# Kernel tuning notes

Hardware: AMD Instinct MI355X
Metric: run time of the kernel (lower is better)

Reference implementation:

```python
import jax, jax.numpy as jnp
import numpy as np

N_SEGMENT = 16
N_HEADS = 12
DIM = 768
HEAD_DIM = DIM // N_HEADS
LN_EPS = 1e-5


def setup_inputs() -> dict:
    key = jax.random.key(0)
    ks = jax.random.split(key, 12)
    nt, p, c = 512, 197, DIM
    s = 1.0 / np.sqrt(c)
    return {
        "x": jax.random.normal(ks[0], (nt, p, c), dtype=jnp.float32),
        "w1": jax.random.uniform(ks[1], (1, 1, c), dtype=jnp.float32) * 2.0 - 1.0,
        "ln_g": jnp.ones((c,), dtype=jnp.float32),
        "ln_b": jnp.zeros((c,), dtype=jnp.float32),
        "Wq": jax.random.normal(ks[2], (c, c), dtype=jnp.float32) * s,
        "bq": jax.random.normal(ks[3], (c,), dtype=jnp.float32) * 0.02,
        "Wk": jax.random.normal(ks[4], (c, c), dtype=jnp.float32) * s,
        "bk": jax.random.normal(ks[5], (c,), dtype=jnp.float32) * 0.02,
        "Wv": jax.random.normal(ks[6], (c, c), dtype=jnp.float32) * s,
        "bv": jax.random.normal(ks[7], (c,), dtype=jnp.float32) * 0.02,
        "Wo": jax.random.normal(ks[8], (c, c), dtype=jnp.float32) * s,
        "bo": jax.random.normal(ks[9], (c,), dtype=jnp.float32) * 0.02,
    }


def _layer_norm(x, g, b):
    mu = jnp.mean(x, axis=-1, keepdims=True)
    var = jnp.mean(jnp.square(x - mu), axis=-1, keepdims=True)
    return (x - mu) * jax.lax.rsqrt(var + LN_EPS) * g + b


def _attention(h, Wq, bq, Wk, bk, Wv, bv, Wo, bo):
    # h: [B, T, C]
    B, T, C = h.shape
    def heads(y):
        return y.reshape(B, T, N_HEADS, HEAD_DIM).transpose(0, 2, 1, 3)
    q = heads(h @ Wq + bq)  # [B, H, T, Dh]
    k = heads(h @ Wk + bk)
    v = heads(h @ Wv + bv)
    scores = jnp.einsum("bhtd,bhsd->bhts", q, k) / jnp.sqrt(jnp.float32(HEAD_DIM))
    probs = jax.nn.softmax(scores, axis=-1)
    ctx = jnp.einsum("bhts,bhsd->bhtd", probs, v)
    ctx = ctx.transpose(0, 2, 1, 3).reshape(B, T, C)
    return ctx @ Wo + bo


def reference(x, w1, ln_g, ln_b, Wq, bq, Wk, bk, Wv, bv, Wo, bo):
    nt, p, c = x.shape
    B = nt // N_SEGMENT
    xr = x.reshape(B, N_SEGMENT, p, c)
    s = xr[:, :, 0]  # CLS tokens [B, T, C]
    # weighted temporal shift (in torch this mutates the view; residual sees it)
    s_shift = s.at[:, 1:].add(s[:, :-1] * w1)
    t = _layer_norm(s_shift, ln_g, ln_b)
    t = _attention(t, Wq, bq, Wk, bk, Wv, bv, Wo, bo)
    t = t + s_shift  # residual uses SHIFTED tokens (aliasing in torch source)
    out = xr.at[:, :, 0].set(t)
    return out.reshape(nt, p, c)
```

## Files before the change

### kernel.cpp

```cpp
#include <hip/hip_runtime.h>
#include <math.h>

typedef __attribute__((ext_vector_type(8))) short short8;
typedef __attribute__((ext_vector_type(4))) float f32x4;
typedef __attribute__((ext_vector_type(4))) unsigned short us4;

constexpr int NSEG = 16;
constexpr int CC   = 768;
constexpr int PP   = 197;
constexpr int NH   = 12;
constexpr int HD   = 64;
constexpr int NT   = 512;
constexpr int MN   = NT * CC;
constexpr float LN_EPS = 1e-5f;

constexpr unsigned CPT  = 196 * CC / 4;
constexpr unsigned TOK4 = PP * CC / 4;
constexpr unsigned ROW4 = CC / 4;
constexpr unsigned W4TOT = (unsigned)NT * CPT;

__device__ inline unsigned short f2bf(float f) {
    unsigned u = __float_as_uint(f);
    u += 0x7fffu + ((u >> 16) & 1u);
    return (unsigned short)(u >> 16);
}

__device__ inline void copy_slice(const float* __restrict__ x, float* __restrict__ out,
                                  unsigned start, unsigned end,
                                  unsigned gthread, unsigned nthreads) {
    const float4* __restrict__ x4 = (const float4*)x;
    float4* __restrict__ o4 = (float4*)out;
    for (unsigned i = start + gthread; i < end; i += nthreads) {
        unsigned t = i / CPT;
        unsigned w = i - t * CPT;
        unsigned idx = t * TOK4 + ROW4 + w;
        o4[idx] = x4[idx];
    }
}

template<bool ADD_RES>
__device__ inline void gemm_tile(const unsigned short* __restrict__ A,
                                 const unsigned short* __restrict__ Bt,
                                 const float* __restrict__ bias,
                                 const float* __restrict__ res,
                                 float* __restrict__ outp,
                                 int by, int bx, size_t orow) {
    int tid  = threadIdx.x;
    int lane = tid & 63, wv = tid >> 6;
    int wr = wv >> 1, wc = wv & 1;
    int l15 = lane & 15, lh = lane >> 4;
    int m0 = by * 64 + wr * 32;
    int n0 = bx * 64 + wc * 32;
    f32x4 acc[2][2] = {};
    const unsigned short* Ar0 = A  + (size_t)(m0 + l15) * CC + lh * 8;
    const unsigned short* Ar1 = Ar0 + 16 * CC;
    const unsigned short* Br0 = Bt + (size_t)(n0 + l15) * CC + lh * 8;
    const unsigned short* Br1 = Br0 + 16 * CC;
    #pragma unroll 4
    for (int k0 = 0; k0 < CC; k0 += 32) {
        short8 a0 = *(const short8*)(Ar0 + k0);
        short8 a1 = *(const short8*)(Ar1 + k0);
        short8 b0 = *(const short8*)(Br0 + k0);
        short8 b1 = *(const short8*)(Br1 + k0);
        acc[0][0] = __builtin_amdgcn_mfma_f32_16x16x32_bf16(a0, b0, acc[0][0], 0, 0, 0);
        acc[0][1] = __builtin_amdgcn_mfma_f32_16x16x32_bf16(a0, b1, acc[0][1], 0, 0, 0);
        acc[1][0] = __builtin_amdgcn_mfma_f32_16x16x32_bf16(a1, b0, acc[1][0], 0, 0, 0);
        acc[1][1] = __builtin_amdgcn_mfma_f32_16x16x32_bf16(a1, b1, acc[1][1], 0, 0, 0);
    }
    #pragma unroll
    for (int mf = 0; mf < 2; ++mf)
        #pragma unroll
        for (int nf = 0; nf < 2; ++nf)
            #pragma unroll
            for (int r = 0; r < 4; ++r) {
                int row = m0 + mf * 16 + lh * 4 + r;
                int col = n0 + nf * 16 + l15;
                float v = acc[mf][nf][r] + bias[col];
                if (ADD_RES) v += res[(size_t)row * CC + col];
                outp[(size_t)row * orow + col] = v;
            }
}

constexpr int K1_LN = NT, K1_CVT = 2304, K1_CPY = 768;
__global__ __launch_bounds__(256) void k1(const float* __restrict__ x, const float* __restrict__ w1,
        const float* __restrict__ g, const float* __restrict__ bln,
        const float* __restrict__ Wq, const float* __restrict__ Wk,
        const float* __restrict__ Wv, const float* __restrict__ Wo,
        float* __restrict__ s_shift, unsigned short* __restrict__ tln,
        unsigned short* __restrict__ wt, float* __restrict__ out,
        unsigned cstart, unsigned cend) {
    __shared__ float smem[32 * 33];
    int bid = blockIdx.x, tid = threadIdx.x;
    if (bid < K1_LN) {
        int r = bid, seg = r & (NSEG - 1);
        float vals[3]; float local = 0.f;
        #pragma unroll
        for (int i = 0; i < 3; ++i) {
            int c = tid + i * 256;
            float v = x[(size_t)r * PP * CC + c];
            if (seg > 0) v += w1[c] * x[(size_t)(r - 1) * PP * CC + c];
            vals[i] = v; local += v;
        }
        smem[tid] = local; __syncthreads();
        for (int off = 128; off > 0; off >>= 1) {
            if (tid < off) smem[tid] += smem[tid + off];
            __syncthreads();
        }
        float mu = smem[0] * (1.0f / CC); __syncthreads();
        float lv = 0.f;
        #pragma unroll
        for (int i = 0; i < 3; ++i) { float d = vals[i] - mu; lv += d * d; }
        smem[tid] = lv; __syncthreads();
        for (int off = 128; off > 0; off >>= 1) {
            if (tid < off) smem[tid] += smem[tid + off];
            __syncthreads();
        }
        float rstd = rsqrtf(smem[0] * (1.0f / CC) + LN_EPS);
        #pragma unroll
        for (int i = 0; i < 3; ++i) {
            int c = tid + i * 256;
            s_shift[(size_t)r * CC + c] = vals[i];
            tln[(size_t)r * CC + c] = f2bf((vals[i] - mu) * rstd * g[c] + bln[c]);
        }
    } else if (bid < K1_LN + K1_CVT) {
        int idx = bid - K1_LN;
        int mat = idx / 576, tile = idx % 576;
        int tr = tile / 24, tc = tile % 24;
        const float* W = mat == 0 ? Wq : mat == 1 ? Wk : mat == 2 ? Wv : Wo;
        int lr = tid >> 3, lc = (tid & 7) * 4;
        float4 v = *(const float4*)(W + (size_t)(tr * 32 + lr) * CC + tc * 32 + lc);
        smem[lr * 33 + lc + 0] = v.x; smem[lr * 33 + lc + 1] = v.y;
        smem[lr * 33 + lc + 2] = v.z; smem[lr * 33 + lc + 3] = v.w;
        __syncthreads();
        int ln_ = tid >> 3, kc = (tid & 7) * 4;
        us4 o;
        #pragma unroll
        for (int j = 0; j < 4; ++j) o[j] = f2bf(smem[(kc + j) * 33 + ln_]);
        *(us4*)(wt + (size_t)mat * CC * CC + (size_t)(tc * 32 + ln_) * CC + tr * 32 + kc) = o;
    } else {
        unsigned cb = bid - (K1_LN + K1_CVT);
        copy_slice(x, out, cstart, cend, cb * 256 + tid, K1_CPY * 256);
    }
}

constexpr int K2_GEMM = 288, K2_CPY = 1024;
__global__ __launch_bounds__(256) void k2(const unsigned short* __restrict__ tln,
        const unsigned short* __restrict__ wt,
        const float* __restrict__ bq, const float* __restrict__ bk, const float* __restrict__ bv,
        float* __restrict__ qkv,
        const float* __restrict__ x, float* __restrict__ out,
        unsigned cstart, unsigned cend) {
    int bid = blockIdx.x, tid = threadIdx.x;
    if (bid < K2_GEMM) {
        int z = bid / 96, rem = bid % 96;
        int by = rem / 12, bx = rem % 12;
        const unsigned short* Bt = wt + (size_t)z * CC * CC;
        const float* bias = z == 0 ? bq : (z == 1 ? bk : bv);
        float* outp = qkv + (size_t)z * MN;
        gemm_tile<false>(tln, Bt, bias, nullptr, outp, by, bx, CC);
    } else {
        unsigned cb = bid - K2_GEMM;
        copy_slice(x, out, cstart, cend, cb * 256 + tid, K2_CPY * 256);
    }
}

constexpr int K3_ATT = 32 * NH, K3_CPY = 1024;
__global__ __launch_bounds__(256) void k3(const float* __restrict__ qkv,
        unsigned short* __restrict__ ctxb,
        const float* __restrict__ x, float* __restrict__ out,
        unsigned cstart, unsigned cend) {
    int bid = blockIdx.x, tid = threadIdx.x;
    if (bid < K3_ATT) {
        const float* q = qkv;
        const float* k = qkv + MN;
        const float* v = qkv + 2 * MN;
        int bb = bid / NH, h = bid % NH;
        __shared__ float qs[16][HD], ks[16][HD], vs[16][HD];
        __shared__ float sc[16][17];
        __shared__ float rsum[16];
        for (int i = tid; i < 16 * HD; i += 256) {
            int t = i >> 6, d = i & 63;
            size_t gidx = (size_t)(bb * NSEG + t) * CC + h * HD + d;
            qs[t][d] = q[gidx]; ks[t][d] = k[gidx]; vs[t][d] = v[gidx];
        }
        __syncthreads();
        {
            int t = tid >> 4, s = tid & 15;
            float acc = 0.f;
            #pragma unroll
            for (int d = 0; d < HD; ++d) acc += qs[t][d] * ks[s][d];
            sc[t][s] = acc * 0.125f;
        }
        __syncthreads();
        if (tid < 16) {
            float m = -1e30f;
            #pragma unroll
            for (int s = 0; s < 16; ++s) m = fmaxf(m, sc[tid][s]);
            float sum = 0.f;
            #pragma unroll
            for (int s = 0; s < 16; ++s) { float e = __expf(sc[tid][s] - m); sc[tid][s] = e; sum += e; }
            rsum[tid] = sum;
        }
        __syncthreads();
        for (int i = tid; i < 16 * HD; i += 256) {
            int t = i >> 6, d = i & 63;
            float acc = 0.f;
            #pragma unroll
            for (int s = 0; s < 16; ++s) acc += sc[t][s] * vs[s][d];
            ctxb[(size_t)(bb * NSEG + t) * CC + h * HD + d] = f2bf(acc / rsum[t]);
        }
    } else {
        unsigned cb = bid - K3_ATT;
        copy_slice(x, out, cstart, cend, cb * 256 + tid, K3_CPY * 256);
    }
}

constexpr int K4_GEMM = 96, K4_CPY = 1024;
__global__ __launch_bounds__(256) void k4(const unsigned short* __restrict__ ctxb,
        const unsigned short* __restrict__ wto,
        const float* __restrict__ bo, const float* __restrict__ s_shift,
        float* __restrict__ out, const float* __restrict__ x,
        unsigned cstart, unsigned cend) {
    int bid = blockIdx.x, tid = threadIdx.x;
    if (bid < K4_GEMM) {
        int by = bid / 12, bx = bid % 12;
        gemm_tile<true>(ctxb, wto, bo, s_shift, out, by, bx, (size_t)PP * CC);
    } else {
        unsigned cb = bid - K4_GEMM;
        copy_slice(x, out, cstart, cend, cb * 256 + tid, K4_CPY * 256);
    }
}

extern "C" void kernel_launch(void* const* d_in, const int* in_sizes, int n_in,
                              void* d_out, int out_size, void* d_ws, size_t ws_size,
                              hipStream_t stream) {
    const float* x    = (const float*)d_in[0];
    const float* w1   = (const float*)d_in[1];
    const float* ln_g = (const float*)d_in[2];
    const float* ln_b = (const float*)d_in[3];
    const float* Wq   = (const float*)d_in[4];
    const float* bq   = (const float*)d_in[5];
    const float* Wk   = (const float*)d_in[6];
    const float* bk   = (const float*)d_in[7];
    const float* Wv   = (const float*)d_in[8];
    const float* bv   = (const float*)d_in[9];
    const float* Wo   = (const float*)d_in[10];
    const float* bo   = (const float*)d_in[11];
    float* out = (float*)d_out;

    float* ws      = (float*)d_ws;
    float* s_shift = ws;
    float* qkv     = s_shift + MN;
    unsigned short* tln  = (unsigned short*)(qkv + 3 * MN);
    unsigned short* ctxb = tln + MN;
    unsigned short* wt   = ctxb + MN;

    const unsigned s0 = 0, s1 = 5400000u, s2 = 10400000u, s3 = 15400000u, s4 = W4TOT;

    k1<<<K1_LN + K1_CVT + K1_CPY, 256, 0, stream>>>(x, w1, ln_g, ln_b, Wq, Wk, Wv, Wo,
                                                    s_shift, tln, wt, out, s0, s1);
    k2<<<K2_GEMM + K2_CPY, 256, 0, stream>>>(tln, wt, bq, bk, bv, qkv, x, out, s1, s2);
    k3<<<K3_ATT + K3_CPY, 256, 0, stream>>>(qkv, ctxb, x, out, s2, s3);
    k4<<<K4_GEMM + K4_CPY, 256, 0, stream>>>(ctxb, wt + (size_t)3 * CC * CC, bo, s_shift,
                                             out, x, s3, s4);
}
```

Baseline: 159.7 us.

## Fuse attention with output projection, store QKV in bf16, rebalance copy across three kernels

Attention and the output projection are merged into one kernel. Each of 32 blocks computes all heads for one batch with wave-level softmax, then runs a per-block MFMA GEMM against Wo. This drops the fourth launch. Q/K/V are now stored as bf16 instead of fp32 to cut intermediate traffic, and weight conversion is done by 576 blocks that each handle all four matrices. The bulk patch-token copy is split into fixed per-block chunks spread over three 2048-block kernels, with occupancy hints in launch bounds. The risks are that the output GEMM now runs on only 32 blocks and that bf16 QKV lowers precision.

```diff
diff --git a/kernel.cpp b/kernel.cpp
--- a/kernel.cpp
+++ b/kernel.cpp
@@ -15,83 +15,45 @@
 constexpr float LN_EPS = 1e-5f;
 
 constexpr unsigned CPT  = 196 * CC / 4;
-constexpr unsigned TOK4 = PP * CC / 4;
 constexpr unsigned ROW4 = CC / 4;
 constexpr unsigned W4TOT = (unsigned)NT * CPT;
+
+constexpr unsigned Q1 = 2944, S1 = 0;
+constexpr unsigned Q2 = 3248, S2 = S1 + 2048u * Q1;
+constexpr unsigned Q3 = 3216, S3 = S2 + 2048u * Q2;
 
 __device__ inline unsigned short f2bf(float f) {
     unsigned u = __float_as_uint(f);
     u += 0x7fffu + ((u >> 16) & 1u);
     return (unsigned short)(u >> 16);
 }
-
-__device__ inline void copy_slice(const float* __restrict__ x, float* __restrict__ out,
-                                  unsigned start, unsigned end,
-                                  unsigned gthread, unsigned nthreads) {
-    const float4* __restrict__ x4 = (const float4*)x;
-    float4* __restrict__ o4 = (float4*)out;
-    for (unsigned i = start + gthread; i < end; i += nthreads) {
-        unsigned t = i / CPT;
-        unsigned w = i - t * CPT;
-        unsigned idx = t * TOK4 + ROW4 + w;
-        o4[idx] = x4[idx];
-    }
-}
-
-template<bool ADD_RES>
-__device__ inline void gemm_tile(const unsigned short* __restrict__ A,
-                                 const unsigned short* __restrict__ Bt,
-                                 const float* __restrict__ bias,
-                                 const float* __restrict__ res,
-                                 float* __restrict__ outp,
-                                 int by, int bx, size_t orow) {
-    int tid  = threadIdx.x;
-    int lane = tid & 63, wv = tid >> 6;
-    int wr = wv >> 1, wc = wv & 1;
-    int l15 = lane & 15, lh = lane >> 4;
-    int m0 = by * 64 + wr * 32;
-    int n0 = bx * 64 + wc * 32;
-    f32x4 acc[2][2] = {};
-    const unsigned short* Ar0 = A  + (size_t)(m0 + l15) * CC + lh * 8;
-    const unsigned short* Ar1 = Ar0 + 16 * CC;
-    const unsigned short* Br0 = Bt + (size_t)(n0 + l15) * CC + lh * 8;
-    const unsigned short* Br1 = Br0 + 16 * CC;
-    #pragma unroll 4
-    for (int k0 = 0; k0 < CC; k0 += 32) {
-        short8 a0 = *(const short8*)(Ar0 + k0);
-        short8 a1 = *(const short8*)(Ar1 + k0);
-        short8 b0 = *(const short8*)(Br0 + k0);
-        short8 b1 = *(const short8*)(Br1 + k0);
-        acc[0][0] = __builtin_amdgcn_mfma_f32_16x16x32_bf16(a0, b0, acc[0][0], 0, 0, 0);
-        acc[0][1] = __builtin_amdgcn_mfma_f32_16x16x32_bf16(a0, b1, acc[0][1], 0, 0, 0);
-        acc[1][0] = __builtin_amdgcn_mfma_f32_16x16x32_bf16(a1, b0, acc[1][0], 0, 0, 0);
-        acc[1][1] = __builtin_amdgcn_mfma_f32_16x16x32_bf16(a1, b1, acc[1][1], 0, 0, 0);
-    }
-    #pragma unroll
-    for (int mf = 0; mf < 2; ++mf)
-        #pragma unroll
-        for (int nf = 0; nf < 2; ++nf)
-            #pragma unroll
-            for (int r = 0; r < 4; ++r) {
-                int row = m0 + mf * 16 + lh * 4 + r;
-                int col = n0 + nf * 16 + l15;
-                float v = acc[mf][nf][r] + bias[col];
-                if (ADD_RES) v += res[(size_t)row * CC + col];
-                outp[(size_t)row * orow + col] = v;
-            }
-}
-
-constexpr int K1_LN = NT, K1_CVT = 2304, K1_CPY = 768;
-__global__ __launch_bounds__(256) void k1(const float* __restrict__ x, const float* __restrict__ w1,
+__device__ inline float bf2f(short v) {
+    return __uint_as_float((unsigned)(unsigned short)v << 16);
+}
+__device__ inline unsigned cidx(unsigned i) {
+    unsigned t = i / CPT;
+    return i + t * ROW4 + ROW4;
+}
+
+__device__ inline void copy_blk(const float* __restrict__ xf, float* __restrict__ of,
+                                unsigned rbeg, unsigned rend, int tid) {
+    const f32x4* __restrict__ x4 = (const f32x4*)xf;
+    f32x4* __restrict__ o4 = (f32x4*)of;
+    for (unsigned i = rbeg + tid; i < rend; i += 256) {
+        unsigned a = cidx(i);
+        o4[a] = x4[a];
+    }
+}
+
+__global__ __launch_bounds__(256, 8) void k1(const float* __restrict__ x, const float* __restrict__ w1,
         const float* __restrict__ g, const float* __restrict__ bln,
         const float* __restrict__ Wq, const float* __restrict__ Wk,
         const float* __restrict__ Wv, const float* __restrict__ Wo,
         float* __restrict__ s_shift, unsigned short* __restrict__ tln,
-        unsigned short* __restrict__ wt, float* __restrict__ out,
-        unsigned cstart, unsigned cend) {
+        unsigned short* __restrict__ wt, float* __restrict__ out) {
     __shared__ float smem[32 * 33];
     int bid = blockIdx.x, tid = threadIdx.x;
-    if (bid < K1_LN) {
+    if (bid < NT) {
         int r = bid, seg = r & (NSEG - 1);
         float vals[3]; float local = 0.f;
         #pragma unroll
@@ -122,113 +84,162 @@
             s_shift[(size_t)r * CC + c] = vals[i];
             tln[(size_t)r * CC + c] = f2bf((vals[i] - mu) * rstd * g[c] + bln[c]);
         }
-    } else if (bid < K1_LN + K1_CVT) {
-        int idx = bid - K1_LN;
-        int mat = idx / 576, tile = idx % 576;
-        int tr = tile / 24, tc = tile % 24;
-        const float* W = mat == 0 ? Wq : mat == 1 ? Wk : mat == 2 ? Wv : Wo;
-        int lr = tid >> 3, lc = (tid & 7) * 4;
-        float4 v = *(const float4*)(W + (size_t)(tr * 32 + lr) * CC + tc * 32 + lc);
-        smem[lr * 33 + lc + 0] = v.x; smem[lr * 33 + lc + 1] = v.y;
-        smem[lr * 33 + lc + 2] = v.z; smem[lr * 33 + lc + 3] = v.w;
-        __syncthreads();
-        int ln_ = tid >> 3, kc = (tid & 7) * 4;
-        us4 o;
-        #pragma unroll
-        for (int j = 0; j < 4; ++j) o[j] = f2bf(smem[(kc + j) * 33 + ln_]);
-        *(us4*)(wt + (size_t)mat * CC * CC + (size_t)(tc * 32 + ln_) * CC + tr * 32 + kc) = o;
-    } else {
-        unsigned cb = bid - (K1_LN + K1_CVT);
-        copy_slice(x, out, cstart, cend, cb * 256 + tid, K1_CPY * 256);
-    }
-}
-
-constexpr int K2_GEMM = 288, K2_CPY = 1024;
-__global__ __launch_bounds__(256) void k2(const unsigned short* __restrict__ tln,
+    } else if (bid < NT + 576) {
+        int bi = bid - NT;
+        int tr = bi / 24, tc = bi % 24;
+        #pragma unroll
+        for (int rep = 0; rep < 4; ++rep) {
+            const float* W = rep == 0 ? Wq : rep == 1 ? Wk : rep == 2 ? Wv : Wo;
+            int lr = tid >> 3, lc = (tid & 7) * 4;
+            float4 v = *(const float4*)(W + (size_t)(tr * 32 + lr) * CC + tc * 32 + lc);
+            smem[lr * 33 + lc + 0] = v.x; smem[lr * 33 + lc + 1] = v.y;
+            smem[lr * 33 + lc + 2] = v.z; smem[lr * 33 + lc + 3] = v.w;
+            __syncthreads();
+            int ln_ = tid >> 3, kc = (tid & 7) * 4;
+            us4 o;
+            #pragma unroll
+            for (int j = 0; j < 4; ++j) o[j] = f2bf(smem[(kc + j) * 33 + ln_]);
+            *(us4*)(wt + (size_t)rep * CC * CC + (size_t)(tc * 32 + ln_) * CC + tr * 32 + kc) = o;
+            __syncthreads();
+        }
+    }
+    copy_blk(x, out, S1 + (unsigned)bid * Q1, S1 + (unsigned)(bid + 1) * Q1, tid);
+}
+
+__global__ __launch_bounds__(256, 4) void k2(const unsigned short* __restrict__ tln,
         const unsigned short* __restrict__ wt,
         const float* __restrict__ bq, const float* __restrict__ bk, const float* __restrict__ bv,
-        float* __restrict__ qkv,
-        const float* __restrict__ x, float* __restrict__ out,
-        unsigned cstart, unsigned cend) {
+        unsigned short* __restrict__ qkvb,
+        const float* __restrict__ x, float* __restrict__ out) {
     int bid = blockIdx.x, tid = threadIdx.x;
-    if (bid < K2_GEMM) {
+    if (bid < 288) {
         int z = bid / 96, rem = bid % 96;
         int by = rem / 12, bx = rem % 12;
         const unsigned short* Bt = wt + (size_t)z * CC * CC;
         const float* bias = z == 0 ? bq : (z == 1 ? bk : bv);
-        float* outp = qkv + (size_t)z * MN;
-        gemm_tile<false>(tln, Bt, bias, nullptr, outp, by, bx, CC);
-    } else {
-        unsigned cb = bid - K2_GEMM;
-        copy_slice(x, out, cstart, cend, cb * 256 + tid, K2_CPY * 256);
-    }
-}
-
-constexpr int K3_ATT = 32 * NH, K3_CPY = 1024;
-__global__ __launch_bounds__(256) void k3(const float* __restrict__ qkv,
-        unsigned short* __restrict__ ctxb,
-        const float* __restrict__ x, float* __restrict__ out,
-        unsigned cstart, unsigned cend) {
-    int bid = blockIdx.x, tid = threadIdx.x;
-    if (bid < K3_ATT) {
-        const float* q = qkv;
-        const float* k = qkv + MN;
-        const float* v = qkv + 2 * MN;
-        int bb = bid / NH, h = bid % NH;
-        __shared__ float qs[16][HD], ks[16][HD], vs[16][HD];
-        __shared__ float sc[16][17];
-        __shared__ float rsum[16];
-        for (int i = tid; i < 16 * HD; i += 256) {
-            int t = i >> 6, d = i & 63;
-            size_t gidx = (size_t)(bb * NSEG + t) * CC + h * HD + d;
-            qs[t][d] = q[gidx]; ks[t][d] = k[gidx]; vs[t][d] = v[gidx];
-        }
-        __syncthreads();
-        {
-            int t = tid >> 4, s = tid & 15;
-            float acc = 0.f;
-            #pragma unroll
-            for (int d = 0; d < HD; ++d) acc += qs[t][d] * ks[s][d];
-            sc[t][s] = acc * 0.125f;
-        }
-        __syncthreads();
-        if (tid < 16) {
-            float m = -1e30f;
-            #pragma unroll
-            for (int s = 0; s < 16; ++s) m = fmaxf(m, sc[tid][s]);
-            float sum = 0.f;
-            #pragma unroll
-            for (int s = 0; s < 16; ++s) { float e = __expf(sc[tid][s] - m); sc[tid][s] = e; sum += e; }
-            rsum[tid] = sum;
-        }
-        __syncthreads();
-        for (int i = tid; i < 16 * HD; i += 256) {
-            int t = i >> 6, d = i & 63;
-            float acc = 0.f;
-            #pragma unroll
-            for (int s = 0; s < 16; ++s) acc += sc[t][s] * vs[s][d];
-            ctxb[(size_t)(bb * NSEG + t) * CC + h * HD + d] = f2bf(acc / rsum[t]);
-        }
-    } else {
-        unsigned cb = bid - K3_ATT;
-        copy_slice(x, out, cstart, cend, cb * 256 + tid, K3_CPY * 256);
-    }
-}
-
-constexpr int K4_GEMM = 96, K4_CPY = 1024;
-__global__ __launch_bounds__(256) void k4(const unsigned short* __restrict__ ctxb,
+        unsigned short* outp = qkvb + (size_t)z * MN;
+        int lane = tid & 63, wv = tid >> 6;
+        int wr = wv >> 1, wc = wv & 1;
+        int l15 = lane & 15, lh = lane >> 4;
+        int m0 = by * 64 + wr * 32;
+        int n0 = bx * 64 + wc * 32;
+        f32x4 acc[2][2] = {};
+        const unsigned short* Ar0 = tln + (size_t)(m0 + l15) * CC + lh * 8;
+        const unsigned short* Ar1 = Ar0 + 16 * CC;
+        const unsigned short* Br0 = Bt + (size_t)(n0 + l15) * CC + lh * 8;
+        const unsigned short* Br1 = Br0 + 16 * CC;
+        #pragma unroll 4
+        for (int k0 = 0; k0 < CC; k0 += 32) {
+            short8 a0 = *(const short8*)(Ar0 + k0);
+            short8 a1 = *(const short8*)(Ar1 + k0);
+            short8 b0 = *(const short8*)(Br0 + k0);
+            short8 b1 = *(const short8*)(Br1 + k0);
+            acc[0][0] = __builtin_amdgcn_mfma_f32_16x16x32_bf16(a0, b0, acc[0][0], 0, 0, 0);
+            acc[0][1] = __builtin_amdgcn_mfma_f32_16x16x32_bf16(a0, b1, acc[0][1], 0, 0, 0);
+            acc[1][0] = __builtin_amdgcn_mfma_f32_16x16x32_bf16(a1, b0, acc[1][0], 0, 0, 0);
+            acc[1][1] = __builtin_amdgcn_mfma_f32_16x16x32_bf16(a1, b1, acc[1][1], 0, 0, 0);
+        }
+        #pragma unroll
+        for (int mf = 0; mf < 2; ++mf)
+            #pragma unroll
+            for (int nf = 0; nf < 2; ++nf)
+                #pragma unroll
+                for (int r = 0; r < 4; ++r) {
+                    int row = m0 + mf * 16 + lh * 4 + r;
+                    int col = n0 + nf * 16 + l15;
+                    outp[(size_t)row * CC + col] = f2bf(acc[mf][nf][r] + bias[col]);
+                }
+    }
+    copy_blk(x, out, S2 + (unsigned)bid * Q2, S2 + (unsigned)(bid + 1) * Q2, tid);
+}
+
+__global__ __launch_bounds__(256, 4) void k3(const unsigned short* __restrict__ qkvb,
         const unsigned short* __restrict__ wto,
         const float* __restrict__ bo, const float* __restrict__ s_shift,
-        float* __restrict__ out, const float* __restrict__ x,
-        unsigned cstart, unsigned cend) {
+        unsigned short* __restrict__ ctxb,
+        float* __restrict__ out, const float* __restrict__ x) {
+    __shared__ float Plds[4][16][17];
     int bid = blockIdx.x, tid = threadIdx.x;
-    if (bid < K4_GEMM) {
-        int by = bid / 12, bx = bid % 12;
-        gemm_tile<true>(ctxb, wto, bo, s_shift, out, by, bx, (size_t)PP * CC);
-    } else {
-        unsigned cb = bid - K4_GEMM;
-        copy_slice(x, out, cstart, cend, cb * 256 + tid, K4_CPY * 256);
-    }
+    if (bid < 32) {
+        int bb = bid;
+        int w = tid >> 6, lane = tid & 63;
+        int t = lane & 15, sg = lane >> 4;
+        const unsigned short* qb = qkvb;
+        const unsigned short* kb = qkvb + MN;
+        const unsigned short* vb = qkvb + 2 * MN;
+        for (int r = 0; r < 3; ++r) {
+            int h = r * 4 + w;
+            const unsigned short* qrow = qb + (size_t)(bb * NSEG + t) * CC + h * HD;
+            const unsigned short* kbase = kb + (size_t)(bb * NSEG) * CC + h * HD;
+            float sc[4] = {0.f, 0.f, 0.f, 0.f};
+            int s0 = sg * 4;
+            for (int c8 = 0; c8 < 8; ++c8) {
+                short8 q8 = *(const short8*)(qrow + c8 * 8);
+                #pragma unroll
+                for (int j = 0; j < 4; ++j) {
+                    short8 k8 = *(const short8*)(kbase + (size_t)(s0 + j) * CC + c8 * 8);
+                    #pragma unroll
+                    for (int e = 0; e < 8; ++e) sc[j] += bf2f(q8[e]) * bf2f(k8[e]);
+                }
+            }
+            #pragma unroll
+            for (int j = 0; j < 4; ++j) sc[j] *= 0.125f;
+            float m = fmaxf(fmaxf(sc[0], sc[1]), fmaxf(sc[2], sc[3]));
+            m = fmaxf(m, __shfl_xor(m, 16));
+            m = fmaxf(m, __shfl_xor(m, 32));
+            float e4[4], ssum = 0.f;
+            #pragma unroll
+            for (int j = 0; j < 4; ++j) { e4[j] = __expf(sc[j] - m); ssum += e4[j]; }
+            ssum += __shfl_xor(ssum, 16);
+            ssum += __shfl_xor(ssum, 32);
+            float inv = 1.f / ssum;
+            #pragma unroll
+            for (int j = 0; j < 4; ++j) Plds[w][t][s0 + j] = e4[j] * inv;
+            int dg = sg;
+            const unsigned short* vbase = vb + (size_t)(bb * NSEG) * CC + h * HD + dg * 16;
+            float o[16];
+            #pragma unroll
+            for (int e = 0; e < 16; ++e) o[e] = 0.f;
+            for (int s = 0; s < 16; ++s) {
+                float p = Plds[w][t][s];
+                short8 va = *(const short8*)(vbase + (size_t)s * CC);
+                short8 vbk = *(const short8*)(vbase + (size_t)s * CC + 8);
+                #pragma unroll
+                for (int e = 0; e < 8; ++e) { o[e] += p * bf2f(va[e]); o[8 + e] += p * bf2f(vbk[e]); }
+            }
+            unsigned short* cdst = ctxb + (size_t)(bb * NSEG + t) * CC + h * HD + dg * 16;
+            #pragma unroll
+            for (int e4i = 0; e4i < 4; ++e4i) {
+                us4 ob;
+                #pragma unroll
+                for (int j = 0; j < 4; ++j) ob[j] = f2bf(o[e4i * 4 + j]);
+                *(us4*)(cdst + e4i * 4) = ob;
+            }
+        }
+        __threadfence_block();
+        __syncthreads();
+        int l15 = lane & 15, lh = lane >> 4;
+        const unsigned short* Arow = ctxb + (size_t)(bb * NSEG + l15) * CC + lh * 8;
+        for (int ti = 0; ti < 12; ++ti) {
+            int n0 = (w + ti * 4) * 16;
+            const unsigned short* Brow = wto + (size_t)(n0 + l15) * CC + lh * 8;
+            f32x4 acc = {0.f, 0.f, 0.f, 0.f};
+            #pragma unroll 4
+            for (int k0 = 0; k0 < CC; k0 += 32) {
+                short8 a = *(const short8*)(Arow + k0);
+                short8 b = *(const short8*)(Brow + k0);
+                acc = __builtin_amdgcn_mfma_f32_16x16x32_bf16(a, b, acc, 0, 0, 0);
+            }
+            #pragma unroll
+            for (int rr = 0; rr < 4; ++rr) {
+                int row = lh * 4 + rr;
+                int col = n0 + l15;
+                float v = acc[rr] + bo[col] + s_shift[(size_t)(bb * NSEG + row) * CC + col];
+                out[(size_t)(bb * NSEG + row) * (size_t)(PP * CC) + col] = v;
+            }
+        }
+    }
+    copy_blk(x, out, S3 + (unsigned)bid * Q3, S3 + (unsigned)(bid + 1) * Q3, tid);
 }
 
 extern "C" void kernel_launch(void* const* d_in, const int* in_sizes, int n_in,
@@ -248,19 +259,13 @@
     const float* bo   = (const float*)d_in[11];
     float* out = (float*)d_out;
 
-    float* ws      = (float*)d_ws;
-    float* s_shift = ws;
-    float* qkv     = s_shift + MN;
-    unsigned short* tln  = (unsigned short*)(qkv + 3 * MN);
-    unsigned short* ctxb = tln + MN;
+    float* s_shift = (float*)d_ws;
+    unsigned short* tln  = (unsigned short*)(s_shift + MN);
+    unsigned short* qkvb = tln + MN;
+    unsigned short* ctxb = qkvb + 3 * (size_t)MN;
     unsigned short* wt   = ctxb + MN;
 
-    const unsigned s0 = 0, s1 = 5400000u, s2 = 10400000u, s3 = 15400000u, s4 = W4TOT;
-
-    k1<<<K1_LN + K1_CVT + K1_CPY, 256, 0, stream>>>(x, w1, ln_g, ln_b, Wq, Wk, Wv, Wo,
-                                                    s_shift, tln, wt, out, s0, s1);
-    k2<<<K2_GEMM + K2_CPY, 256, 0, stream>>>(tln, wt, bq, bk, bv, qkv, x, out, s1, s2);
-    k3<<<K3_ATT + K3_CPY, 256, 0, stream>>>(qkv, ctxb, x, out, s2, s3);
-    k4<<<K4_GEMM + K4_CPY, 256, 0, stream>>>(ctxb, wt + (size_t)3 * CC * CC, bo, s_shift,
-                                             out, x, s3, s4);
-}
+    k1<<<2048, 256, 0, stream>>>(x, w1, ln_g, ln_b, Wq, Wk, Wv, Wo, s_shift, tln, wt, out);
+    k2<<<2048, 256, 0, stream>>>(tln, wt, bq, bk, bv, qkvb, x, out);
+    k3<<<2048, 256, 0, stream>>>(qkvb, wt + (size_t)3 * CC * CC, bo, s_shift, ctxb, out, x);
+}
```

Measured after the change: 248.3 us. +55.4%, slower.
